# Kernel tuning notes

Measured on AMD Instinct MI355X. Metric: run time of the kernel, lower is better.

The kernel has to match this reference:

```python
import jax, jax.numpy as jnp
import numpy as np

H = 1024       # hidden_size
R = 4          # downsacale_ratio -> bottleneck H//R = 256
DI = 2048      # mamba d_inner = expand * H
NS = 16        # d_state
KC = 4         # d_conv
DTR = 64       # dt_rank = ceil(H/16)
B, L = 4, 1024


def setup_inputs() -> dict:
    key = jax.random.key(0)
    ks = iter(jax.random.split(key, 32))
    w = lambda shape, s=0.02: jax.random.normal(next(ks), shape, jnp.float32) * s
    Hr = H // R
    inp = {
        'x': jax.random.normal(next(ks), (B, L, H), jnp.float32),
        't': jax.random.normal(next(ks), (B, H), jnp.float32),
        # adaLN modulation: SiLU -> Linear(H, 3H)
        'ada_w': w((H, 3 * H)), 'ada_b': jnp.zeros((3 * H,), jnp.float32),
        # hg_dense: Linear(H,H/R) SiLU Linear(H/R,H)
        'hgd_w1': w((H, Hr)), 'hgd_b1': jnp.zeros((Hr,), jnp.float32),
        'hgd_w2': w((Hr, H)), 'hgd_b2': jnp.zeros((H,), jnp.float32),
        # Mamba params
        'in_proj_w': w((H, 2 * DI)),
        'conv_w': w((DI, KC), 0.1), 'conv_b': jnp.zeros((DI,), jnp.float32),
        'x_proj_w': w((DI, DTR + 2 * NS)),
        'dt_proj_w': w((DTR, DI), 0.1),
        'dt_proj_b': jnp.log(jnp.expm1(jnp.full((DI,), 0.01, jnp.float32))),  # softplus^-1(0.01)
        'A_log': jnp.log(jnp.broadcast_to(jnp.arange(1, NS + 1, dtype=jnp.float32), (DI, NS))),
        'Dp': jnp.ones((DI,), jnp.float32),
        'out_proj_w': w((DI, H)),
        # hg_fuse
        'fm_w': w((H, Hr)), 'fm_b': jnp.zeros((Hr,), jnp.float32),
        'fr_w': w((H, Hr)), 'fr_b': jnp.zeros((Hr,), jnp.float32),
        'ff_w': w((Hr, H)), 'ff_b': jnp.zeros((H,), jnp.float32),
    }
    return inp


def _ln(x, eps=1e-6):
    mu = jnp.mean(x, -1, keepdims=True)
    var = jnp.mean(jnp.square(x - mu), -1, keepdims=True)
    return (x - mu) / jnp.sqrt(var + eps)


def _mamba(xd, in_proj_w, conv_w, conv_b, x_proj_w, dt_proj_w, dt_proj_b, A_log, Dp, out_proj_w):
    # xd: [B, L, H]
    xz = xd @ in_proj_w                      # [B, L, 2*DI]
    xm, z = jnp.split(xz, 2, axis=-1)
    # causal depthwise conv over time
    xc = jnp.swapaxes(xm, 1, 2)              # [B, DI, L]
    xc = jax.lax.conv_general_dilated(
        xc, conv_w[:, None, :], window_strides=(1,), padding=[(KC - 1, 0)],
        feature_group_count=DI, dimension_numbers=('NCH', 'OIH', 'NCH'))
    xc = jax.nn.silu(jnp.swapaxes(xc, 1, 2) + conv_b)   # [B, L, DI]
    dbl = xc @ x_proj_w                      # [B, L, DTR + 2*NS]
    dt = jax.nn.softplus(dbl[..., :DTR] @ dt_proj_w + dt_proj_b)   # [B, L, DI]
    Bm = dbl[..., DTR:DTR + NS]              # [B, L, NS]
    Cm = dbl[..., DTR + NS:]                 # [B, L, NS]
    A = -jnp.exp(A_log)                      # [DI, NS]

    def step(h, inp):
        dt_t, x_t, B_t, C_t = inp            # [B,DI],[B,DI],[B,NS],[B,NS]
        dA = jnp.exp(dt_t[:, :, None] * A)                       # [B, DI, NS]
        h = dA * h + (dt_t * x_t)[:, :, None] * B_t[:, None, :]
        y = jnp.einsum('bdn,bn->bd', h, C_t)
        return h, y

    h0 = jnp.zeros((xd.shape[0], DI, NS), xd.dtype)
    seq = (jnp.moveaxis(dt, 1, 0), jnp.moveaxis(xc, 1, 0),
           jnp.moveaxis(Bm, 1, 0), jnp.moveaxis(Cm, 1, 0))
    _, ys = jax.lax.scan(step, h0, seq)
    y = jnp.moveaxis(ys, 0, 1) + xc * Dp     # [B, L, DI]
    y = y * jax.nn.silu(z)
    return y @ out_proj_w                    # [B, L, H]


def reference(x, t, ada_w, ada_b, hgd_w1, hgd_b1, hgd_w2, hgd_b2,
              in_proj_w, conv_w, conv_b, x_proj_w, dt_proj_w, dt_proj_b,
              A_log, Dp, out_proj_w, fm_w, fm_b, fr_w, fr_b, ff_w, ff_b):
    ada = jax.nn.silu(t) @ ada_w + ada_b               # [B, 3H]
    shift, scale, alpha = jnp.split(ada, 3, axis=-1)
    x1 = _ln(x) * (1 + scale[:, None, :]) + shift[:, None, :]
    xd = jax.nn.silu(x1 @ hgd_w1 + hgd_b1) @ hgd_w2 + hgd_b2
    x1_2 = _mamba(xd, in_proj_w, conv_w, conv_b, x_proj_w, dt_proj_w,
                  dt_proj_b, A_log, Dp, out_proj_w)
    a = jax.nn.silu(x1_2 @ fm_w + fm_b)
    b = jax.nn.silu(x1 @ fr_w + fr_b)
    fuse = (a * b) @ ff_w + ff_b
    return x + alpha[:, None, :] * fuse
```

## Files before the change

kernel.cpp:

```cpp
#include <hip/hip_runtime.h>
#include <math.h>
#include <stdint.h>

#define H_   1024
#define HR_  256
#define DI_  2048
#define NS_  16
#define KC_  4
#define DTR_ 64
#define B_   4
#define L_   1024
#define ROWS (B_*L_)
#define H3_  3072
#define NCH_ 16
#define CL_  64
#define CLT_ 8

typedef short bf16x8 __attribute__((ext_vector_type(8)));
typedef float f32x4  __attribute__((ext_vector_type(4)));

__device__ __forceinline__ float silu_f(float v) { return v / (1.f + __expf(-v)); }

__device__ __forceinline__ uint32_t pack_bf16_2(float a, float b) {
    uint32_t ua = __float_as_uint(a);
    uint32_t ub = __float_as_uint(b);
    uint32_t ra = (ua + 0x7FFFu + ((ua >> 16) & 1u)) >> 16;
    uint32_t rb = (ub + 0x7FFFu + ((ub >> 16) & 1u)) >> 16;
    return ra | (rb << 16);
}
__device__ __forceinline__ unsigned short cvt_bf16(float a) {
    uint32_t ua = __float_as_uint(a);
    return (unsigned short)((ua + 0x7FFFu + ((ua >> 16) & 1u)) >> 16);
}
__device__ __forceinline__ float bf16_to_f(unsigned short u) {
    return __uint_as_float(((uint32_t)u) << 16);
}

__device__ __forceinline__ void gload16(const short* g, short* l) {
    __builtin_amdgcn_global_load_lds(
        (const __attribute__((address_space(1))) void*)g,
        (__attribute__((address_space(3))) void*)l, 16, 0, 0);
}

#define TW_HGDFR 0ull
#define TW_HGD2  524288ull
#define TW_INPJ  786432ull
#define TW_XPJ   4980736ull
#define TW_DTPJ  5242880ull
#define TW_OPJ   5373952ull
#define TW_FM    7471104ull
#define TW_FF    7733248ull
#define TWT      7995392ull

__global__ __launch_bounds__(256) void wtrans_kernel(
    const float* __restrict__ s0, const float* __restrict__ s1,
    const float* __restrict__ s2, const float* __restrict__ s3,
    const float* __restrict__ s4, const float* __restrict__ s5,
    const float* __restrict__ s6, const float* __restrict__ s7,
    const float* __restrict__ s8, short* __restrict__ wt)
{
    int bid = blockIdx.x;
    const float* src; short* dst; int K, N, rel;
    if      (bid < 256)  { src = s0; dst = wt + TW_HGDFR;          K = 1024; N = 256;  rel = bid; }
    else if (bid < 512)  { src = s1; dst = wt + TW_HGDFR + 262144; K = 1024; N = 256;  rel = bid - 256; }
    else if (bid < 768)  { src = s2; dst = wt + TW_HGD2;           K = 256;  N = 1024; rel = bid - 512; }
    else if (bid < 4864) { src = s3; dst = wt + TW_INPJ;           K = 1024; N = 4096; rel = bid - 768; }
    else if (bid < 5120) { src = s4; dst = wt + TW_XPJ;            K = 2048; N = 96;   rel = bid - 4864; }
    else if (bid < 5248) { src = s5; dst = wt + TW_DTPJ;           K = 64;   N = 2048; rel = bid - 5120; }
    else if (bid < 7296) { src = s6; dst = wt + TW_OPJ;            K = 2048; N = 1024; rel = bid - 5248; }
    else if (bid < 7552) { src = s7; dst = wt + TW_FM;             K = 1024; N = 256;  rel = bid - 7296; }
    else                 { src = s8; dst = wt + TW_FF;             K = 256;  N = 1024; rel = bid - 7552; }
    int tkc = K >> 5;
    int tk = rel % tkc, tn = rel / tkc;

    __shared__ float ld[32][33];
    int tx = threadIdx.x & 7, ty = threadIdx.x >> 3;
    int kk = tk * 32 + ty, nn = tn * 32 + tx * 4;
    float4 v = make_float4(0.f, 0.f, 0.f, 0.f);
    if (nn < N) v = *(const float4*)&src[(size_t)kk * N + nn];
    ld[ty][tx * 4 + 0] = v.x; ld[ty][tx * 4 + 1] = v.y;
    ld[ty][tx * 4 + 2] = v.z; ld[ty][tx * 4 + 3] = v.w;
    __syncthreads();
    int nn2 = tn * 32 + ty, kk2 = tk * 32 + tx * 4;
    float a0 = ld[tx * 4 + 0][ty], a1 = ld[tx * 4 + 1][ty];
    float a2 = ld[tx * 4 + 2][ty], a3 = ld[tx * 4 + 3][ty];
    uint2 p = { pack_bf16_2(a0, a1), pack_bf16_2(a2, a3) };
    *(uint2*)&dst[(size_t)nn2 * K + kk2] = p;
}

__global__ __launch_bounds__(256) void cwt_kernel(
    const float* __restrict__ conv_w, float* __restrict__ cwt)
{
    int d = blockIdx.x * 256 + threadIdx.x;
    float4 v = *(const float4*)&conv_w[d * KC_];
    cwt[0 * DI_ + d] = v.x;
    cwt[1 * DI_ + d] = v.y;
    cwt[2 * DI_ + d] = v.z;
    cwt[3 * DI_ + d] = v.w;
}

__global__ __launch_bounds__(256) void ada_kernel(
    const float* __restrict__ t, const float* __restrict__ ada_w,
    const float* __restrict__ ada_b, float* __restrict__ ada)
{
    int b   = blockIdx.y;
    int col = blockIdx.x * 256 + threadIdx.x;
    __shared__ float st[H_];
    for (int i = threadIdx.x; i < H_; i += 256) {
        float v = t[b * H_ + i];
        st[i] = silu_f(v);
    }
    __syncthreads();
    float acc = 0.f;
    for (int k = 0; k < H_; ++k)
        acc = fmaf(st[k], ada_w[(size_t)k * H3_ + col], acc);
    ada[b * H3_ + col] = acc + ada_b[col];
}

__global__ __launch_bounds__(256) void ln_mod_kernel(
    const float* __restrict__ x, const float* __restrict__ ada,
    short* __restrict__ x1b)
{
    int row = blockIdx.x;
    int b   = row >> 10;
    const float* xr = x + (size_t)row * H_;
    float4 v = ((const float4*)xr)[threadIdx.x];
    float s  = v.x + v.y + v.z + v.w;
    float s2 = v.x*v.x + v.y*v.y + v.z*v.z + v.w*v.w;

    __shared__ float red[8];
    int wave = threadIdx.x >> 6, lane = threadIdx.x & 63;
    #pragma unroll
    for (int off = 32; off; off >>= 1) {
        s  += __shfl_down(s,  off);
        s2 += __shfl_down(s2, off);
    }
    if (lane == 0) { red[wave] = s; red[4 + wave] = s2; }
    __syncthreads();
    float ts  = red[0] + red[1] + red[2] + red[3];
    float ts2 = red[4] + red[5] + red[6] + red[7];
    float mu  = ts  * (1.f / H_);
    float var = ts2 * (1.f / H_) - mu * mu;
    float inv = rsqrtf(var + 1e-6f);

    const float* sh = ada + b * H3_;
    int i = threadIdx.x * 4;
    float4 sh4 = *(const float4*)&sh[i];
    float4 sc4 = *(const float4*)&sh[H_ + i];
    float ox = (v.x - mu) * inv * (1.f + sc4.x) + sh4.x;
    float oy = (v.y - mu) * inv * (1.f + sc4.y) + sh4.y;
    float oz = (v.z - mu) * inv * (1.f + sc4.z) + sh4.z;
    float ow = (v.w - mu) * inv * (1.f + sc4.w) + sh4.w;
    uint2 p = { pack_bf16_2(ox, oy), pack_bf16_2(oz, ow) };
    *(uint2*)(x1b + (size_t)row * H_ + i) = p;
}

template<int ACT, bool SPLITK>
__global__ __launch_bounds__(256) void gemm128(
    const short* __restrict__ A, int lda,
    const short* __restrict__ Wt, int ldw,
    const float* __restrict__ bias,
    float* __restrict__ C, short* __restrict__ Cb, short* __restrict__ Cb2,
    int ldc, int M, int N, int K,
    const float* __restrict__ E0, const float* __restrict__ E1)
{
    __shared__ short As[3][4096];
    __shared__ short Bs[3][4096];
    int tid  = threadIdx.x;
    int lane = tid & 63, wv = tid >> 6, wm = wv >> 1, wn = wv & 1;
    int n0 = blockIdx.x * 128;
    int m0 = blockIdx.y * 128;

    if (SPLITK) {
        int z = blockIdx.z;
        A  += (size_t)z * K;
        Wt += (size_t)z * K;
        C  += (size_t)z * M * N;
    }

    int r = lane & 15, g = lane >> 4;
    int sA = wv * 2;
    const short* ga0 = A  + (size_t)(m0 + sA * 16 + r) * lda + g * 8;
    const short* ga1 = ga0 + (size_t)16 * lda;
    const short* gb0 = Wt + (size_t)(n0 + sA * 16 + r) * ldw + g * 8;
    const short* gb1 = gb0 + (size_t)16 * ldw;

    f32x4 acc[4][4];
    #pragma unroll
    for (int i = 0; i < 4; ++i)
        #pragma unroll
        for (int j = 0; j < 4; ++j) {
            acc[i][j][0] = 0.f; acc[i][j][1] = 0.f;
            acc[i][j][2] = 0.f; acc[i][j][3] = 0.f;
        }

    #define STAGE(buf, koff)                                    \
        do {                                                    \
            gload16(ga0 + (koff), &As[buf][sA * 512]);          \
            gload16(ga1 + (koff), &As[buf][sA * 512 + 512]);    \
            gload16(gb0 + (koff), &Bs[buf][sA * 512]);          \
            gload16(gb1 + (koff), &Bs[buf][sA * 512 + 512]);    \
        } while (0)

    #define COMPUTE(buf)                                                          \
        do {                                                                      \
            bf16x8 af[4], bfr[4];                                                 \
            _Pragma("unroll")                                                     \
            for (int i = 0; i < 4; ++i)                                           \
                af[i] = *(const bf16x8*)&As[buf][(wm * 4 + i) * 512 + lane * 8];  \
            _Pragma("unroll")                                                     \
            for (int j = 0; j < 4; ++j)                                           \
                bfr[j] = *(const bf16x8*)&Bs[buf][(wn * 4 + j) * 512 + lane * 8]; \
            _Pragma("unroll")                                                     \
            for (int i = 0; i < 4; ++i)                                           \
                _Pragma("unroll")                                                 \
                for (int j = 0; j < 4; ++j)                                       \
                    acc[i][j] = __builtin_amdgcn_mfma_f32_16x16x32_bf16(          \
                        af[i], bfr[j], acc[i][j], 0, 0, 0);                       \
        } while (0)

    int T = K >> 5;
    STAGE(0, 0);
    if (T > 1) STAGE(1, 32);
    for (int t = 0; t < T; ++t) {
        if (t + 1 < T) asm volatile("s_waitcnt vmcnt(4)" ::: "memory");
        else           asm volatile("s_waitcnt vmcnt(0)" ::: "memory");
        __builtin_amdgcn_s_barrier();
        if (t + 2 < T) STAGE((t + 2) % 3, (t + 2) * 32);
        COMPUTE(t % 3);
    }
    #undef STAGE
    #undef COMPUTE

    #pragma unroll
    for (int i = 0; i < 4; ++i) {
        int mb = m0 + wm * 64 + i * 16 + ((lane >> 4) << 2);
        #pragma unroll
        for (int j = 0; j < 4; ++j) {
            int n = n0 + wn * 64 + j * 16 + (lane & 15);
            if (n < N) {
                float bv;
                if (ACT == 6) bv = (n < 256) ? bias[n] : E0[n - 256];
                else          bv = bias ? bias[n] : 0.f;
                #pragma unroll
                for (int rr = 0; rr < 4; ++rr) {
                    int m = mb + rr;
                    float v = acc[i][j][rr] + bv;
                    size_t ci = (size_t)m * ldc + n;
                    if (ACT == 6) {
                        float sv = silu_f(v);
                        if (n < 256) Cb[(size_t)m * 256 + n]        = (short)cvt_bf16(sv);
                        else         Cb2[(size_t)m * 256 + (n-256)] = (short)cvt_bf16(sv);
                    } else {
                        if (ACT == 2) v = (v > 20.f) ? v : log1pf(__expf(v));
                        else if (ACT == 4) {
                            int bb = m >> 10;
                            v = E0[ci] + E1[bb * H3_ + 2 * H_ + n] * v;
                        }
                        if (C)  C[ci]  = v;
                        if (Cb) Cb[ci] = (short)cvt_bf16(v);
                    }
                }
            }
        }
    }
}

template<int ACT>
__global__ __launch_bounds__(512) void gemm256(
    const short* __restrict__ A, int lda,
    const short* __restrict__ Wt, int ldw,
    short* __restrict__ Cb, int M, int N, int K)
{
    extern __shared__ short lds[];
    short* Asb = lds;
    short* Bsb = lds + 24576;
    int tid  = threadIdx.x;
    int lane = tid & 63, wv = tid >> 6;
    int wm = wv >> 2, wn = wv & 3;
    int n0 = blockIdx.x * 256;
    int m0 = blockIdx.y * 256;

    int r = lane & 15, g = lane >> 4;
    int sA = wv * 2;
    const short* ga0 = A  + (size_t)(m0 + sA * 16 + r) * lda + g * 8;
    const short* ga1 = ga0 + (size_t)16 * lda;
    const short* gb0 = Wt + (size_t)(n0 + sA * 16 + r) * ldw + g * 8;
    const short* gb1 = gb0 + (size_t)16 * ldw;

    f32x4 acc[8][4];
    #pragma unroll
    for (int i = 0; i < 8; ++i)
        #pragma unroll
        for (int j = 0; j < 4; ++j) {
            acc[i][j][0] = 0.f; acc[i][j][1] = 0.f;
            acc[i][j][2] = 0.f; acc[i][j][3] = 0.f;
        }

    #define STAGE2(buf, koff)                                       \
        do {                                                        \
            gload16(ga0 + (koff), &Asb[(buf) * 8192 + sA * 512]);   \
            gload16(ga1 + (koff), &Asb[(buf) * 8192 + sA * 512 + 512]); \
            gload16(gb0 + (koff), &Bsb[(buf) * 8192 + sA * 512]);   \
            gload16(gb1 + (koff), &Bsb[(buf) * 8192 + sA * 512 + 512]); \
        } while (0)

    int T = K >> 5;
    STAGE2(0, 0);
    if (T > 1) STAGE2(1, 32);
    for (int t = 0; t < T; ++t) {
        if (t + 1 < T) asm volatile("s_waitcnt vmcnt(4)" ::: "memory");
        else           asm volatile("s_waitcnt vmcnt(0)" ::: "memory");
        __builtin_amdgcn_s_barrier();
        if (t + 2 < T) STAGE2((t + 2) % 3, (t + 2) * 32);
        {
            int buf = t % 3;
            bf16x8 af[8], bfr[4];
            #pragma unroll
            for (int i = 0; i < 8; ++i)
                af[i] = *(const bf16x8*)&Asb[buf * 8192 + (wm * 8 + i) * 512 + lane * 8];
            #pragma unroll
            for (int j = 0; j < 4; ++j)
                bfr[j] = *(const bf16x8*)&Bsb[buf * 8192 + (wn * 4 + j) * 512 + lane * 8];
            __builtin_amdgcn_s_setprio(1);
            #pragma unroll
            for (int i = 0; i < 8; ++i)
                #pragma unroll
                for (int j = 0; j < 4; ++j)
                    acc[i][j] = __builtin_amdgcn_mfma_f32_16x16x32_bf16(
                        af[i], bfr[j], acc[i][j], 0, 0, 0);
            __builtin_amdgcn_s_setprio(0);
        }
    }
    #undef STAGE2

    #pragma unroll
    for (int i = 0; i < 8; ++i) {
        int mb = m0 + wm * 128 + i * 16 + ((lane >> 4) << 2);
        #pragma unroll
        for (int j = 0; j < 4; ++j) {
            int n = n0 + wn * 64 + j * 16 + (lane & 15);
            #pragma unroll
            for (int rr = 0; rr < 4; ++rr) {
                int m = mb + rr;
                float v = acc[i][j][rr];
                if (ACT == 5) {
                    size_t idx = (n < DI_) ? ((size_t)m * DI_ + n)
                                           : ((size_t)ROWS * DI_ + (size_t)m * DI_ + (n - DI_));
                    Cb[idx] = (short)cvt_bf16(v);
                }
            }
        }
    }
}

__global__ __launch_bounds__(256) void redk_xproj(
    const float* __restrict__ part, float* __restrict__ dbl,
    short* __restrict__ dblb)
{
    size_t i = ((size_t)blockIdx.x * 256 + threadIdx.x) * 4;
    const size_t seg = (size_t)ROWS * 96;
    float4 s = *(const float4*)(part + i);
    #pragma unroll
    for (int z = 1; z < 8; ++z) {
        float4 p = *(const float4*)(part + z * seg + i);
        s.x += p.x; s.y += p.y; s.z += p.z; s.w += p.w;
    }
    *(float4*)(dbl + i) = s;
    uint2 p = { pack_bf16_2(s.x, s.y), pack_bf16_2(s.z, s.w) };
    *(uint2*)(dblb + i) = p;
}

__global__ __launch_bounds__(256) void redk_op(
    const float* __restrict__ part, short* __restrict__ x12b)
{
    size_t i = ((size_t)blockIdx.x * 256 + threadIdx.x) * 4;
    const size_t seg = (size_t)ROWS * H_;
    float4 a = *(const float4*)(part + i);
    float4 b = *(const float4*)(part + seg + i);
    uint2 p = { pack_bf16_2(a.x + b.x, a.y + b.y), pack_bf16_2(a.z + b.z, a.w + b.w) };
    *(uint2*)(x12b + i) = p;
}

__global__ __launch_bounds__(256) void redk_fm(
    const float* __restrict__ part, const float* __restrict__ fm_b,
    const short* __restrict__ frlin, short* __restrict__ abb)
{
    size_t i = ((size_t)blockIdx.x * 256 + threadIdx.x) * 4;
    const size_t seg = (size_t)ROWS * HR_;
    float4 s = *(const float4*)(part + i);
    #pragma unroll
    for (int z = 1; z < 4; ++z) {
        float4 p = *(const float4*)(part + z * seg + i);
        s.x += p.x; s.y += p.y; s.z += p.z; s.w += p.w;
    }
    int col = (int)(i & (HR_ - 1));
    float4 b = *(const float4*)(fm_b + col);
    const short* fr = frlin + i;
    float o0 = silu_f(s.x + b.x) * bf16_to_f((unsigned short)fr[0]);
    float o1 = silu_f(s.y + b.y) * bf16_to_f((unsigned short)fr[1]);
    float o2 = silu_f(s.z + b.z) * bf16_to_f((unsigned short)fr[2]);
    float o3 = silu_f(s.w + b.w) * bf16_to_f((unsigned short)fr[3]);
    uint2 p = { pack_bf16_2(o0, o1), pack_bf16_2(o2, o3) };
    *(uint2*)(abb + i) = p;
}

__global__ __launch_bounds__(256) void conv_kernel(
    const short* __restrict__ xmb, const float* __restrict__ cwt,
    const float* __restrict__ conv_b, short* __restrict__ xcb)
{
    int d0 = threadIdx.x * 8;
    int b  = blockIdx.y;
    int l0 = blockIdx.x * CLT_;

    float w[KC_][8];
    #pragma unroll
    for (int j = 0; j < KC_; ++j) {
        float4 a = *(const float4*)&cwt[j * DI_ + d0];
        float4 c = *(const float4*)&cwt[j * DI_ + d0 + 4];
        w[j][0] = a.x; w[j][1] = a.y; w[j][2] = a.z; w[j][3] = a.w;
        w[j][4] = c.x; w[j][5] = c.y; w[j][6] = c.z; w[j][7] = c.w;
    }
    float bia[8];
    {
        float4 b0 = *(const float4*)&conv_b[d0];
        float4 b1 = *(const float4*)&conv_b[d0 + 4];
        bia[0] = b0.x; bia[1] = b0.y; bia[2] = b0.z; bia[3] = b0.w;
        bia[4] = b1.x; bia[5] = b1.y; bia[6] = b1.z; bia[7] = b1.w;
    }

    const short* base = xmb + (size_t)b * L_ * DI_ + d0;
    short*       outb = xcb + (size_t)b * L_ * DI_ + d0;

    bf16x8 win[KC_];
    #pragma unroll
    for (int j = 0; j < KC_ - 1; ++j) {
        int ll = l0 - (KC_ - 1) + j;
        if (ll >= 0) win[j] = *(const bf16x8*)(base + (size_t)ll * DI_);
        else         win[j] = (bf16x8)0;
    }
    for (int l = l0; l < l0 + CLT_; ++l) {
        win[KC_ - 1] = *(const bf16x8*)(base + (size_t)l * DI_);
        bf16x8 o;
        #pragma unroll
        for (int e = 0; e < 8; ++e) {
            float acc = bia[e];
            #pragma unroll
            for (int j = 0; j < KC_; ++j)
                acc = fmaf(bf16_to_f((unsigned short)win[j][e]), w[j][e], acc);
            o[e] = (short)cvt_bf16(silu_f(acc));
        }
        *(bf16x8*)(outb + (size_t)l * DI_) = o;
        win[0] = win[1]; win[1] = win[2]; win[2] = win[3];
    }
}

__global__ __launch_bounds__(256) void scan_part1(
    const short* __restrict__ dtb, const short* __restrict__ xcb,
    const float* __restrict__ dbl, const float* __restrict__ A_log,
    float* __restrict__ hend, float* __restrict__ dtsum)
{
    int bx = blockIdx.x;
    int dg = bx & 15;
    int bc = bx >> 4;
    int c  = bc & (NCH_ - 1);
    int b  = bc >> 4;
    int tid  = threadIdx.x;
    int d    = dg * 128 + (tid >> 1);
    int half = tid & 1;
    int n0   = half * 8;

    float Aa[8];
    #pragma unroll
    for (int n = 0; n < 8; ++n) Aa[n] = -__expf(A_log[d * NS_ + n0 + n]);

    __shared__ float sB[CL_][NS_];
    for (int idx = threadIdx.x; idx < CL_ * NS_; idx += 256) {
        int l = idx >> 4, n = idx & 15;
        sB[l][n] = dbl[(size_t)(b * L_ + c * CL_ + l) * 96 + DTR_ + n];
    }
    __syncthreads();

    float h[8];
    #pragma unroll
    for (int n = 0; n < 8; ++n) h[n] = 0.f;
    float sdt = 0.f;

    for (int l = 0; l < CL_; ++l) {
        size_t off = (size_t)(b * L_ + c * CL_ + l) * DI_ + d;
        float dtv = bf16_to_f((unsigned short)dtb[off]);
        float xv  = bf16_to_f((unsigned short)xcb[off]);
        float du  = dtv * xv;
        sdt += dtv;
        #pragma unroll
        for (int n = 0; n < 8; ++n)
            h[n] = fmaf(__expf(dtv * Aa[n]), h[n], du * sB[l][n0 + n]);
    }
    #pragma unroll
    for (int n = 0; n < 8; ++n)
        hend[((size_t)((b * NCH_ + c) * NS_ + n0 + n)) * DI_ + d] = h[n];
    if (half == 0)
        dtsum[(size_t)(b * NCH_ + c) * DI_ + d] = sdt;
}

__global__ __launch_bounds__(256) void scan_mid(
    const float* __restrict__ hend, const float* __restrict__ dtsum,
    const float* __restrict__ A_log, float* __restrict__ hin)
{
    int idx = blockIdx.x * 256 + threadIdx.x;
    int d  = idx & (DI_ - 1);
    int bn = idx >> 11;
    int n  = bn & (NS_ - 1);
    int b  = bn >> 4;
    float Aa = -__expf(A_log[d * NS_ + n]);
    float h = 0.f;
    #pragma unroll
    for (int c = 0; c < NCH_; ++c) {
        size_t o = ((size_t)((b * NCH_ + c) * NS_ + n)) * DI_ + d;
        hin[o] = h;
        float s = dtsum[(size_t)(b * NCH_ + c) * DI_ + d];
        h = fmaf(__expf(Aa * s), h, hend[o]);
    }
}

__global__ __launch_bounds__(256) void scan_part2(
    const short* __restrict__ dtb, const short* __restrict__ xcb,
    const short* __restrict__ zb, const float* __restrict__ dbl,
    const float* __restrict__ A_log, const float* __restrict__ Dp,
    const float* __restrict__ hin, short* __restrict__ y2b)
{
    int bx = blockIdx.x;
    int dg = bx & 15;
    int bc = bx >> 4;
    int c  = bc & (NCH_ - 1);
    int b  = bc >> 4;
    int tid  = threadIdx.x;
    int d    = dg * 128 + (tid >> 1);
    int half = tid & 1;
    int n0   = half * 8;

    float Aa[8];
    #pragma unroll
    for (int n = 0; n < 8; ++n) Aa[n] = -__expf(A_log[d * NS_ + n0 + n]);

    __shared__ float sBC[CL_][2 * NS_];
    for (int idx = threadIdx.x; idx < CL_ * 2 * NS_; idx += 256) {
        int l = idx >> 5, n = idx & 31;
        sBC[l][n] = dbl[(size_t)(b * L_ + c * CL_ + l) * 96 + DTR_ + n];
    }
    __syncthreads();

    float h[8];
    #pragma unroll
    for (int n = 0; n < 8; ++n)
        h[n] = hin[((size_t)((b * NCH_ + c) * NS_ + n0 + n)) * DI_ + d];

    float Dpv = Dp[d];
    for (int l = 0; l < CL_; ++l) {
        size_t row = (size_t)(b * L_ + c * CL_ + l);
        size_t off = row * DI_ + d;
        float dtv = bf16_to_f((unsigned short)dtb[off]);
        float xv  = bf16_to_f((unsigned short)xcb[off]);
        float zv  = bf16_to_f((unsigned short)zb[off]);
        float du  = dtv * xv;
        float y = 0.f;
        #pragma unroll
        for (int n = 0; n < 8; ++n) {
            float dA = __expf(dtv * Aa[n]);
            h[n] = fmaf(dA, h[n], du * sBC[l][n0 + n]);
            y = fmaf(h[n], sBC[l][NS_ + n0 + n], y);
        }
        y += __shfl_xor(y, 1);
        if (half == 0) {
            y = fmaf(xv, Dpv, y);
            y2b[off] = (short)cvt_bf16(y * silu_f(zv));
        }
    }
}

extern "C" void kernel_launch(void* const* d_in, const int* in_sizes, int n_in,
                              void* d_out, int out_size, void* d_ws, size_t ws_size,
                              hipStream_t stream)
{
    const float* x         = (const float*)d_in[0];
    const float* t         = (const float*)d_in[1];
    const float* ada_w     = (const float*)d_in[2];
    const float* ada_b     = (const float*)d_in[3];
    const float* hgd_w1    = (const float*)d_in[4];
    const float* hgd_b1    = (const float*)d_in[5];
    const float* hgd_w2    = (const float*)d_in[6];
    const float* hgd_b2    = (const float*)d_in[7];
    const float* in_proj_w = (const float*)d_in[8];
    const float* conv_w    = (const float*)d_in[9];
    const float* conv_b    = (const float*)d_in[10];
    const float* x_proj_w  = (const float*)d_in[11];
    const float* dt_proj_w = (const float*)d_in[12];
    const float* dt_proj_b = (const float*)d_in[13];
    const float* A_log     = (const float*)d_in[14];
    const float* Dp        = (const float*)d_in[15];
    const float* out_proj_w= (const float*)d_in[16];
    const float* fm_w      = (const float*)d_in[17];
    const float* fm_b      = (const float*)d_in[18];
    const float* fr_w      = (const float*)d_in[19];
    const float* fr_b      = (const float*)d_in[20];
    const float* ff_w      = (const float*)d_in[21];
    const float* ff_b      = (const float*)d_in[22];
    float* out = (float*)d_out;

    char* p = (char*)d_ws;
    auto alloc = [&](size_t bytes) { char* r = p; p += (bytes + 255) & ~255ull; return r; };

    short* wt      = (short*)alloc(TWT * 2);
    float* cwt     = (float*)alloc((size_t)KC_ * DI_ * 4);
    short* x1b     = (short*)alloc((size_t)ROWS * H_ * 2);
    short* h1b     = (short*)alloc((size_t)ROWS * HR_ * 2);
    short* frlin   = (short*)alloc((size_t)ROWS * HR_ * 2);
    short* xdb     = (short*)alloc((size_t)ROWS * H_ * 2);
    short* xmzb    = (short*)alloc((size_t)ROWS * DI_ * 4);
    short* xcb     = (short*)alloc((size_t)ROWS * DI_ * 2);
    short* y2b     = (short*)alloc((size_t)ROWS * DI_ * 2);
    short* dtb     = (short*)alloc((size_t)ROWS * DI_ * 2);
    float* bigpart = (float*)alloc((size_t)2 * ROWS * H_ * 4);
    float* dbl     = (float*)alloc((size_t)ROWS * 96 * 4);
    short* dblb    = (short*)alloc((size_t)ROWS * 96 * 2);
    short* x12b    = (short*)alloc((size_t)ROWS * H_ * 2);
    short* abb     = (short*)alloc((size_t)ROWS * HR_ * 2);
    float* ada     = (float*)alloc((size_t)B_ * H3_ * 4);

    short* xmb   = xmzb;
    short* zb    = xmzb + (size_t)ROWS * DI_;
    float* hend  = (float*)x12b;
    float* dtsum = (float*)abb;
    float* hin   = bigpart;

    dim3 blk(256), b512(512);

    wtrans_kernel<<<dim3(7808), blk, 0, stream>>>(
        hgd_w1, fr_w, hgd_w2, in_proj_w, x_proj_w, dt_proj_w, out_proj_w,
        fm_w, ff_w, wt);
    cwt_kernel<<<dim3(DI_ / 256), blk, 0, stream>>>(conv_w, cwt);
    ada_kernel<<<dim3(H3_ / 256, B_), blk, 0, stream>>>(t, ada_w, ada_b, ada);
    ln_mod_kernel<<<dim3(ROWS), blk, 0, stream>>>(x, ada, x1b);
    gemm128<6, false><<<dim3(4, 32), blk, 0, stream>>>(
        x1b, H_, wt + TW_HGDFR, H_, hgd_b1, nullptr, h1b, frlin,
        512, ROWS, 512, H_, fr_b, nullptr);
    gemm128<0, false><<<dim3(8, 32), blk, 0, stream>>>(
        h1b, HR_, wt + TW_HGD2, HR_, hgd_b2, nullptr, xdb, nullptr,
        H_, ROWS, H_, HR_, nullptr, nullptr);
    gemm256<5><<<dim3(16, 16), b512, 98304, stream>>>(
        xdb, H_, wt + TW_INPJ, H_, xmb, ROWS, 2 * DI_, H_);
    conv_kernel<<<dim3(L_ / CLT_, B_), blk, 0, stream>>>(xmb, cwt, conv_b, xcb);
    gemm128<0, true><<<dim3(1, 32, 8), blk, 0, stream>>>(
        xcb, DI_, wt + TW_XPJ, DI_, nullptr, bigpart, nullptr, nullptr,
        96, ROWS, 96, 256, nullptr, nullptr);
    redk_xproj<<<dim3(ROWS * 96 / 4 / 256), blk, 0, stream>>>(bigpart, dbl, dblb);
    gemm128<2, false><<<dim3(16, 32), blk, 0, stream>>>(
        dblb, 96, wt + TW_DTPJ, DTR_, dt_proj_b, nullptr, dtb, nullptr,
        DI_, ROWS, DI_, DTR_, nullptr, nullptr);
    scan_part1<<<dim3(B_ * NCH_ * 16), blk, 0, stream>>>(
        dtb, xcb, dbl, A_log, hend, dtsum);
    scan_mid<<<dim3(B_ * DI_ * NS_ / 256), blk, 0, stream>>>(
        hend, dtsum, A_log, hin);
    scan_part2<<<dim3(B_ * NCH_ * 16), blk, 0, stream>>>(
        dtb, xcb, zb, dbl, A_log, Dp, hin, y2b);
    gemm128<0, true><<<dim3(8, 32, 2), blk, 0, stream>>>(
        y2b, DI_, wt + TW_OPJ, DI_, nullptr, bigpart, nullptr, nullptr,
        H_, ROWS, H_, 1024, nullptr, nullptr);
    redk_op<<<dim3(ROWS * H_ / 4 / 256), blk, 0, stream>>>(bigpart, x12b);
    gemm128<0, true><<<dim3(2, 32, 4), blk, 0, stream>>>(
        x12b, H_, wt + TW_FM, H_, nullptr, bigpart, nullptr, nullptr,
        HR_, ROWS, HR_, 256, nullptr, nullptr);
    redk_fm<<<dim3(ROWS * HR_ / 4 / 256), blk, 0, stream>>>(bigpart, fm_b, frlin, abb);
    gemm128<4, false><<<dim3(8, 32), blk, 0, stream>>>(
        abb, HR_, wt + TW_FF, HR_, ff_b, out, nullptr, nullptr,
        H_, ROWS, H_, HR_, x, ada);
}
```

Measured before the change: 409.0 us.

## Double-buffer dt/xc/z tiles into LDS with async loads in scan kernels

The chunked scan kernels now stage 16-timestep tiles of dt, xc (and z in part2) into shared memory with 16-byte global-to-LDS loads, double-buffered so the next tile loads while the current one is scanned. Previously each thread issued dependent 2-byte global loads per timestep inside the serial recurrence, which exposed memory latency. The change adds LDS usage and extra barriers per tile, and relies on an existing gload16 helper for the async copy.

```diff
diff --git a/kernel.cpp b/kernel.cpp
--- a/kernel.cpp
+++ b/kernel.cpp
@@ -466,36 +466,61 @@
     int c  = bc & (NCH_ - 1);
     int b  = bc >> 4;
     int tid  = threadIdx.x;
-    int d    = dg * 128 + (tid >> 1);
+    int lane = tid & 63, wv = tid >> 6;
+    int dl   = tid >> 1;
+    int d    = dg * 128 + dl;
     int half = tid & 1;
     int n0   = half * 8;
 
-    float Aa[8];
-    #pragma unroll
-    for (int n = 0; n < 8; ++n) Aa[n] = -__expf(A_log[d * NS_ + n0 + n]);
-
     __shared__ float sB[CL_][NS_];
-    for (int idx = threadIdx.x; idx < CL_ * NS_; idx += 256) {
+    __shared__ short dtS[2][16][128];
+    __shared__ short xcS[2][16][128];
+
+    size_t srcoff = (size_t)(b * L_ + c * CL_ + wv * 4 + (lane >> 4)) * DI_
+                    + dg * 128 + (lane & 15) * 8;
+    const short* gdt = dtb + srcoff;
+    const short* gxc = xcb + srcoff;
+
+    #define SSTG1(buf, q)                                             \
+        do {                                                          \
+            gload16(gdt + (size_t)(q) * 16 * DI_, &dtS[buf][wv*4][0]); \
+            gload16(gxc + (size_t)(q) * 16 * DI_, &xcS[buf][wv*4][0]); \
+        } while (0)
+
+    SSTG1(0, 0);
+    for (int idx = tid; idx < CL_ * NS_; idx += 256) {
         int l = idx >> 4, n = idx & 15;
         sB[l][n] = dbl[(size_t)(b * L_ + c * CL_ + l) * 96 + DTR_ + n];
     }
-    __syncthreads();
+    float Aa[8];
+    #pragma unroll
+    for (int n = 0; n < 8; ++n) Aa[n] = -__expf(A_log[d * NS_ + n0 + n]);
 
     float h[8];
     #pragma unroll
     for (int n = 0; n < 8; ++n) h[n] = 0.f;
     float sdt = 0.f;
 
-    for (int l = 0; l < CL_; ++l) {
-        size_t off = (size_t)(b * L_ + c * CL_ + l) * DI_ + d;
-        float dtv = bf16_to_f((unsigned short)dtb[off]);
-        float xv  = bf16_to_f((unsigned short)xcb[off]);
-        float du  = dtv * xv;
-        sdt += dtv;
+    __syncthreads();
+    int buf = 0;
+    for (int q = 0; q < 4; ++q) {
+        if (q < 3) SSTG1(buf ^ 1, q + 1);
         #pragma unroll
-        for (int n = 0; n < 8; ++n)
-            h[n] = fmaf(__expf(dtv * Aa[n]), h[n], du * sB[l][n0 + n]);
-    }
+        for (int li = 0; li < 16; ++li) {
+            int l = q * 16 + li;
+            float dtv = bf16_to_f((unsigned short)dtS[buf][li][dl]);
+            float xv  = bf16_to_f((unsigned short)xcS[buf][li][dl]);
+            float du  = dtv * xv;
+            sdt += dtv;
+            #pragma unroll
+            for (int n = 0; n < 8; ++n)
+                h[n] = fmaf(__expf(dtv * Aa[n]), h[n], du * sB[l][n0 + n]);
+        }
+        __syncthreads();
+        buf ^= 1;
+    }
+    #undef SSTG1
+
     #pragma unroll
     for (int n = 0; n < 8; ++n)
         hend[((size_t)((b * NCH_ + c) * NS_ + n0 + n)) * DI_ + d] = h[n];
@@ -535,47 +560,74 @@
     int c  = bc & (NCH_ - 1);
     int b  = bc >> 4;
     int tid  = threadIdx.x;
-    int d    = dg * 128 + (tid >> 1);
+    int lane = tid & 63, wv = tid >> 6;
+    int dl   = tid >> 1;
+    int d    = dg * 128 + dl;
     int half = tid & 1;
     int n0   = half * 8;
 
-    float Aa[8];
-    #pragma unroll
-    for (int n = 0; n < 8; ++n) Aa[n] = -__expf(A_log[d * NS_ + n0 + n]);
-
     __shared__ float sBC[CL_][2 * NS_];
-    for (int idx = threadIdx.x; idx < CL_ * 2 * NS_; idx += 256) {
+    __shared__ short dtS[2][16][128];
+    __shared__ short xcS[2][16][128];
+    __shared__ short zS[2][16][128];
+
+    size_t srcoff = (size_t)(b * L_ + c * CL_ + wv * 4 + (lane >> 4)) * DI_
+                    + dg * 128 + (lane & 15) * 8;
+    const short* gdt = dtb + srcoff;
+    const short* gxc = xcb + srcoff;
+    const short* gz  = zb  + srcoff;
+
+    #define SSTG2(buf, q)                                             \
+        do {                                                          \
+            gload16(gdt + (size_t)(q) * 16 * DI_, &dtS[buf][wv*4][0]); \
+            gload16(gxc + (size_t)(q) * 16 * DI_, &xcS[buf][wv*4][0]); \
+            gload16(gz  + (size_t)(q) * 16 * DI_, &zS[buf][wv*4][0]);  \
+        } while (0)
+
+    SSTG2(0, 0);
+    for (int idx = tid; idx < CL_ * 2 * NS_; idx += 256) {
         int l = idx >> 5, n = idx & 31;
         sBC[l][n] = dbl[(size_t)(b * L_ + c * CL_ + l) * 96 + DTR_ + n];
     }
-    __syncthreads();
+    float Aa[8];
+    #pragma unroll
+    for (int n = 0; n < 8; ++n) Aa[n] = -__expf(A_log[d * NS_ + n0 + n]);
 
     float h[8];
     #pragma unroll
     for (int n = 0; n < 8; ++n)
         h[n] = hin[((size_t)((b * NCH_ + c) * NS_ + n0 + n)) * DI_ + d];
-
     float Dpv = Dp[d];
-    for (int l = 0; l < CL_; ++l) {
-        size_t row = (size_t)(b * L_ + c * CL_ + l);
-        size_t off = row * DI_ + d;
-        float dtv = bf16_to_f((unsigned short)dtb[off]);
-        float xv  = bf16_to_f((unsigned short)xcb[off]);
-        float zv  = bf16_to_f((unsigned short)zb[off]);
-        float du  = dtv * xv;
-        float y = 0.f;
+    size_t obase = (size_t)(b * L_ + c * CL_) * DI_ + d;
+
+    __syncthreads();
+    int buf = 0;
+    for (int q = 0; q < 4; ++q) {
+        if (q < 3) SSTG2(buf ^ 1, q + 1);
         #pragma unroll
-        for (int n = 0; n < 8; ++n) {
-            float dA = __expf(dtv * Aa[n]);
-            h[n] = fmaf(dA, h[n], du * sBC[l][n0 + n]);
-            y = fmaf(h[n], sBC[l][NS_ + n0 + n], y);
+        for (int li = 0; li < 16; ++li) {
+            int l = q * 16 + li;
+            float dtv = bf16_to_f((unsigned short)dtS[buf][li][dl]);
+            float xv  = bf16_to_f((unsigned short)xcS[buf][li][dl]);
+            float zv  = bf16_to_f((unsigned short)zS[buf][li][dl]);
+            float du  = dtv * xv;
+            float y = 0.f;
+            #pragma unroll
+            for (int n = 0; n < 8; ++n) {
+                float dA = __expf(dtv * Aa[n]);
+                h[n] = fmaf(dA, h[n], du * sBC[l][n0 + n]);
+                y = fmaf(h[n], sBC[l][NS_ + n0 + n], y);
+            }
+            y += __shfl_xor(y, 1);
+            if (half == 0) {
+                y = fmaf(xv, Dpv, y);
+                y2b[obase + (size_t)l * DI_] = (short)cvt_bf16(y * silu_f(zv));
+            }
         }
-        y += __shfl_xor(y, 1);
-        if (half == 0) {
-            y = fmaf(xv, Dpv, y);
-            y2b[off] = (short)cvt_bf16(y * silu_f(zv));
-        }
-    }
+        __syncthreads();
+        buf ^= 1;
+    }
+    #undef SSTG2
 }
 
 extern "C" void kernel_launch(void* const* d_in, const int* in_sizes, int n_in,
```

After: 388.2 us. 5.1% less time.
